# Performance work log

Hardware: AMD Instinct MI355X
Metric: run time of the kernel (lower is better)

## Reference

```python
import jax, jax.numpy as jnp
import numpy as np

B, C, H, W = 8, 32, 512, 512
WS = 8
CQ = C // 4                      # 8
N = (H // WS) * (W // WS)        # 4096 windows
ED = WS * WS * C                 # 2048 embed_dim
EPS = 1e-6


def setup_inputs() -> dict:
    key = jax.random.key(0)
    ks = jax.random.split(key, 16)
    s = 0.02
    return {
        "input_x": jax.random.normal(ks[0], (B, C, H, W), jnp.float32),
        # in_conv: Conv2d(C, C//4, 1)
        "w_in": jax.random.normal(ks[1], (CQ, C), jnp.float32) * s,
        "b_in": jnp.zeros((CQ,), jnp.float32),
        # conv: Conv2d(C, C//4, 1) + LayerNorm(C//4)
        "w_conv": jax.random.normal(ks[2], (CQ, C), jnp.float32) * s,
        "b_conv": jnp.zeros((CQ,), jnp.float32),
        "ln_w": jnp.ones((CQ,), jnp.float32),
        "ln_b": jnp.zeros((CQ,), jnp.float32),
        # out_CA: Conv2d(C//4, C, 1)
        "w_ca": jax.random.normal(ks[3], (C, CQ), jnp.float32) * s,
        "b_ca": jnp.zeros((C,), jnp.float32),
        # out_SA: Conv2d(C//4, 1, 3, pad 1)
        "w_sa": jax.random.normal(ks[4], (1, CQ, 3, 3), jnp.float32) * s,
        "b_sa": jnp.zeros((1,), jnp.float32),
        # out_mask MLP: Linear(ED, ED//2), Linear(ED//2, ED)  (torch weight [out,in])
        "w_m1": jax.random.normal(ks[5], (ED // 2, ED), jnp.float32) * s,
        "b_m1": jnp.zeros((ED // 2,), jnp.float32),
        "w_m2": jax.random.normal(ks[6], (ED, ED // 2), jnp.float32) * s,
        "b_m2": jnp.zeros((ED,), jnp.float32),
    }


def _leaky(x):
    return jax.nn.leaky_relu(x, 0.1)


def _conv1x1(x, w, b):
    # x: [B,Cin,H,W], w: [Cout,Cin]
    return jnp.einsum('bchw,oc->bohw', x, w) + b[None, :, None, None]


def reference(input_x, w_in, b_in, w_conv, b_conv, ln_w, ln_b,
              w_ca, b_ca, w_sa, b_sa, w_m1, b_m1, w_m2, b_m2):
    b_, c_, h_, w_ = input_x.shape
    n_win = (h_ // WS) * (w_ // WS)

    # in_conv branch
    x = _leaky(_conv1x1(input_x, w_in, b_in))          # [B,CQ,H,W]

    # conv branch: 1x1 conv -> channels_first LayerNorm -> leaky
    x_ = _conv1x1(input_x, w_conv, b_conv)             # [B,CQ,H,W]
    u = jnp.mean(x_, axis=1, keepdims=True)
    s = jnp.mean((x_ - u) ** 2, axis=1, keepdims=True)
    x_ = (x_ - u) / jnp.sqrt(s + EPS)
    x_ = _leaky(ln_w[None, :, None, None] * x_ + ln_b[None, :, None, None])

    # channel attention: global avg pool -> 1x1 conv -> sigmoid
    pooled = jnp.mean(x_, axis=(2, 3), keepdims=True)  # [B,CQ,1,1]
    ca = jax.nn.sigmoid(_conv1x1(pooled, w_ca, b_ca))  # [B,C,1,1]

    # spatial attention: 3x3 conv -> sigmoid
    sa = jax.lax.conv_general_dilated(
        x_, w_sa, (1, 1), 'SAME',
        dimension_numbers=('NCHW', 'OIHW', 'NCHW')) + b_sa[None, :, None, None]
    sa = jax.nn.sigmoid(sa)                            # [B,1,H,W]

    # window variance + bottom-k mask
    xm = jnp.mean(x, axis=1)                           # [B,H,W]
    xw = xm.reshape(b_, h_ // WS, WS, w_ // WS, WS)
    xw = xw.transpose(0, 1, 3, 2, 4).reshape(b_, n_win, WS * WS)  # [B,N,64]
    var_x = jnp.var(xw, axis=-1, ddof=1)               # [B,N] (torch unbiased var)
    k_top = n_win // 2
    _, idx = jax.lax.top_k(-var_x, k_top)              # indices of smallest-variance windows
    mask = jnp.ones((b_, n_win), input_x.dtype)
    mask = mask.at[jnp.arange(b_)[:, None], idx].set(0.0)  # vectorized scatter

    # broadcast 0/1 mask across embed dim, then MLP (see notes re: original bug)
    m = jnp.broadcast_to(mask[:, :, None], (b_, n_win, w_m1.shape[1]))
    hdd = _leaky(jnp.einsum('bnd,ed->bne', m, w_m1) + b_m1)
    out_mask = jnp.einsum('bne,fe->bnf', hdd, w_m2) + b_m2  # [B,N,ED]

    return (out_mask, ca, sa)
```

## Files before the change

kernel.cpp:

```cpp
#include <hip/hip_runtime.h>
#include <math.h>

#define B_   8
#define C_   32
#define H_   512
#define W_   512
#define CQ_  8
#define NW_  4096
#define ED_  2048
#define EH_  1024
#define EPS_ 1e-6f

#define AS1 __attribute__((address_space(1)))
#define AS3 __attribute__((address_space(3)))

__device__ __forceinline__ float leaky(float x) { return x > 0.f ? x : 0.1f * x; }
__device__ __forceinline__ float sigmoidf_(float x) { return 1.f / (1.f + __expf(-x)); }

__global__ __launch_bounds__(1024, 4) void pass_a(
    const float* __restrict__ x,
    const float* __restrict__ w_in, const float* __restrict__ b_in,
    const float* __restrict__ w_conv, const float* __restrict__ b_conv,
    const float* __restrict__ ln_w, const float* __restrict__ ln_b,
    float* __restrict__ xq_out,
    double* __restrict__ var_out,
    float* __restrict__ pooled_part)
{
    __shared__ float stage[3][4096];
    __shared__ float xm[4096];
    __shared__ float red[16][CQ_];

    const int tid  = threadIdx.x;
    const int band = blockIdx.x;
    const int b    = blockIdx.y;
    const int lane = tid & 63, wv = tid >> 6;
    const size_t plane = (size_t)H_ * W_;
    const float* xb = x + (size_t)b * C_ * plane;
    const float* gw = xb + (size_t)band * (8 * W_) + wv * 256 + lane * 4;

#define STAGE(buf, c)                                                          \
    __builtin_amdgcn_global_load_lds(                                          \
        (const AS1 unsigned int*)(gw + (size_t)(c) * plane),                   \
        (AS3 unsigned int*)(&stage[buf][wv * 256]), 16, 0, 0);

    float ycv[CQ_][4], yin[CQ_][4];
#pragma unroll
    for (int q = 0; q < CQ_; ++q)
#pragma unroll
        for (int j = 0; j < 4; ++j) { ycv[q][j] = 0.f; yin[q][j] = 0.f; }

    STAGE(0, 0) STAGE(1, 1) STAGE(2, 2)

#pragma unroll
    for (int c = 0; c < C_; ++c) {
        if (c < 30)       asm volatile("s_waitcnt vmcnt(2)" ::: "memory");
        else if (c == 30) asm volatile("s_waitcnt vmcnt(1)" ::: "memory");
        else              asm volatile("s_waitcnt vmcnt(0)" ::: "memory");
        asm volatile("s_barrier" ::: "memory");

        const float4 v = *reinterpret_cast<const float4*>(&stage[c % 3][tid * 4]);
#pragma unroll
        for (int q = 0; q < CQ_; ++q) {
            const float wc = w_conv[q * C_ + c];
            const float wi = w_in[q * C_ + c];
            ycv[q][0] = fmaf(wc, v.x, ycv[q][0]);
            ycv[q][1] = fmaf(wc, v.y, ycv[q][1]);
            ycv[q][2] = fmaf(wc, v.z, ycv[q][2]);
            ycv[q][3] = fmaf(wc, v.w, ycv[q][3]);
            yin[q][0] = fmaf(wi, v.x, yin[q][0]);
            yin[q][1] = fmaf(wi, v.y, yin[q][1]);
            yin[q][2] = fmaf(wi, v.z, yin[q][2]);
            yin[q][3] = fmaf(wi, v.w, yin[q][3]);
        }
        asm volatile("s_waitcnt lgkmcnt(0)" ::: "memory");
        asm volatile("s_barrier" ::: "memory");
        if (c + 3 < C_) { STAGE(c % 3, c + 3) }
    }
#undef STAGE

#pragma unroll
    for (int q = 0; q < CQ_; ++q) {
        const float bc = b_conv[q];
#pragma unroll
        for (int j = 0; j < 4; ++j) ycv[q][j] += bc;
    }

    float ps[CQ_];
#pragma unroll
    for (int q = 0; q < CQ_; ++q) ps[q] = 0.f;

    float xmv[4];
#pragma unroll
    for (int j = 0; j < 4; ++j) {
        float u = 0.f;
#pragma unroll
        for (int q = 0; q < CQ_; ++q) u += ycv[q][j];
        u *= 0.125f;
        float s = 0.f;
#pragma unroll
        for (int q = 0; q < CQ_; ++q) { const float d = ycv[q][j] - u; s = fmaf(d, d, s); }
        s *= 0.125f;
        const float inv = 1.f / sqrtf(s + EPS_);
        float m = 0.f;
#pragma unroll
        for (int q = 0; q < CQ_; ++q) {
            const float xv = leaky(fmaf(ln_w[q], (ycv[q][j] - u) * inv, ln_b[q]));
            ycv[q][j] = xv;
            ps[q] += xv;
            m += leaky(yin[q][j] + b_in[q]);
        }
        xmv[j] = m * 0.125f;
    }

    const int py = tid >> 7, px = (tid & 127) * 4;

#pragma unroll
    for (int q = 0; q < CQ_; ++q) {
        *reinterpret_cast<float4*>(
            &xq_out[(((size_t)b * CQ_ + q) * H_ + band * 8 + py) * W_ + px]) =
            make_float4(ycv[q][0], ycv[q][1], ycv[q][2], ycv[q][3]);
    }

    *reinterpret_cast<float4*>(&xm[tid * 4]) = make_float4(xmv[0], xmv[1], xmv[2], xmv[3]);

#pragma unroll
    for (int q = 0; q < CQ_; ++q) {
        float s = ps[q];
#pragma unroll
        for (int off = 32; off; off >>= 1) s += __shfl_xor(s, off);
        if (lane == 0) red[wv][q] = s;
    }

    __syncthreads();

    if (tid < CQ_) {
        float s = 0.f;
#pragma unroll
        for (int w = 0; w < 16; ++w) s += red[w][tid];
        const int bid = blockIdx.y * gridDim.x + blockIdx.x;
        pooled_part[bid * CQ_ + tid] = s;
    }

#pragma unroll
    for (int k = 0; k < 4; ++k) {
        const int win = wv * 4 + k;
        const double dv = (double)xm[(lane >> 3) * 512 + win * 8 + (lane & 7)];
        double s = dv;
#pragma unroll
        for (int off = 32; off; off >>= 1) s += __shfl_xor(s, off);
        const double mean = s * (1.0 / 64.0);
        const double d = dv - mean;
        double s2 = d * d;
#pragma unroll
        for (int off = 32; off; off >>= 1) s2 += __shfl_xor(s2, off);
        if (lane == 0) {
            const int n = band * 64 + win;
            var_out[(size_t)b * NW_ + n] = s2 * (1.0 / 63.0);
        }
    }
}

__global__ __launch_bounds__(256) void sa_kernel(
    const float* __restrict__ xq,
    const float* __restrict__ w_sa, const float* __restrict__ b_sa,
    float* __restrict__ sa_out)
{
    __shared__ float xl[CQ_][18][72];
    const int tid = threadIdx.x;
    const int b = blockIdx.z;
    const int ty = blockIdx.y * 16, tx = blockIdx.x * 64;

    for (int idx = tid; idx < CQ_ * 18 * 18; idx += 256) {
        const int ch = idx / 324;
        const int rem = idx % 324;
        const int r = rem / 18, c4 = rem % 18;
        const int gy = ty + r - 1;
        const int gxf = tx + c4 * 4 - 4;
        float4 v = make_float4(0.f, 0.f, 0.f, 0.f);
        if (gy >= 0 && gy < H_ && gxf >= 0 && gxf < W_)
            v = *reinterpret_cast<const float4*>(
                    &xq[(((size_t)b * CQ_ + ch) * H_ + gy) * W_ + gxf]);
        *reinterpret_cast<float4*>(&xl[ch][r][c4 * 4]) = v;
    }
    __syncthreads();

    const int px = (tid & 15) * 4, py = tid >> 4;
    const float bsa = b_sa[0];
    float acc[4] = {bsa, bsa, bsa, bsa};
#pragma unroll
    for (int q = 0; q < CQ_; ++q) {
#pragma unroll
        for (int dy = 0; dy < 3; ++dy) {
            const float* r = &xl[q][py + dy][px];
            const float4 aa = *reinterpret_cast<const float4*>(r);
            const float4 bb = *reinterpret_cast<const float4*>(r + 4);
            const float4 cc = *reinterpret_cast<const float4*>(r + 8);
            const float a[12] = {aa.x, aa.y, aa.z, aa.w, bb.x, bb.y, bb.z, bb.w,
                                 cc.x, cc.y, cc.z, cc.w};
#pragma unroll
            for (int dx = 0; dx < 3; ++dx) {
                const float w = w_sa[q * 9 + dy * 3 + dx];
#pragma unroll
                for (int j = 0; j < 4; ++j) acc[j] = fmaf(w, a[j + 3 + dx], acc[j]);
            }
        }
    }
    const float4 o = make_float4(sigmoidf_(acc[0]), sigmoidf_(acc[1]),
                                 sigmoidf_(acc[2]), sigmoidf_(acc[3]));
    *reinterpret_cast<float4*>(&sa_out[((size_t)b * H_ + (ty + py)) * W_ + tx + px]) = o;
}

__global__ __launch_bounds__(256) void k2_kernel(
    const double* __restrict__ var, float* __restrict__ maskF,
    const float* __restrict__ w_m1, const float* __restrict__ b_m1,
    float* __restrict__ h1, float* __restrict__ h0,
    const float* __restrict__ pooled_part,
    const float* __restrict__ w_ca, const float* __restrict__ b_ca,
    float* __restrict__ ca_out)
{
    __shared__ double sv[NW_];
    const int bi = blockIdx.x;
    const int tid = threadIdx.x;

    if (bi < 128) {
        const int b = bi >> 4;
        const double* vb = var + (size_t)b * NW_;
        for (int j = tid; j < NW_; j += 256) sv[j] = vb[j];
        __syncthreads();
        const int i = (bi & 15) * 256 + tid;
        const double vi = sv[i];
        int cnt = 0;
#pragma unroll 4
        for (int j = 0; j < NW_; ++j) {
            const double vj = sv[j];
            cnt += (vj < vi) || (vj == vi && j < i);
        }
        maskF[(size_t)b * NW_ + i] = (cnt < NW_ / 2) ? 0.f : 1.f;
    } else if (bi < 384) {
        const int wave = tid >> 6, lane = tid & 63;
        const int e = (bi - 128) * 4 + wave;
        const float* row = w_m1 + (size_t)e * ED_;
        float s = 0.f;
#pragma unroll
        for (int k = 0; k < ED_ / 64; ++k) s += row[lane + 64 * k];
#pragma unroll
        for (int off = 32; off; off >>= 1) s += __shfl_xor(s, off);
        if (lane == 0) {
            h1[e] = leaky(s + b_m1[e]);
            h0[e] = leaky(b_m1[e]);
        }
    } else {
        float* sp = (float*)sv;
        const int bq = tid >> 2, part = tid & 3;
        const int bb = bq >> 3, q = bq & 7;
        float s = 0.f;
        for (int k = part; k < 64; k += 4) s += pooled_part[((size_t)bb * 64 + k) * CQ_ + q];
        sp[tid] = s;
        __syncthreads();
        if (tid < 64)
            sp[256 + tid] = (sp[4 * tid] + sp[4 * tid + 1] + sp[4 * tid + 2] + sp[4 * tid + 3])
                            * (1.f / ((float)H_ * (float)W_));
        __syncthreads();
        const int ob = tid >> 5, o = tid & 31;
        float acc = b_ca[o];
#pragma unroll
        for (int qq = 0; qq < CQ_; ++qq)
            acc = fmaf(w_ca[o * CQ_ + qq], sp[256 + ob * CQ_ + qq], acc);
        ca_out[tid] = sigmoidf_(acc);
    }
}

__global__ __launch_bounds__(256) void o_kernel(const float* __restrict__ w_m2,
                                                const float* __restrict__ b_m2,
                                                const float* __restrict__ h1,
                                                const float* __restrict__ h0,
                                                float* __restrict__ o1, float* __restrict__ o0)
{
    const int wave = threadIdx.x >> 6, lane = threadIdx.x & 63;
    const int f = blockIdx.x * 4 + wave;
    const float* row = w_m2 + (size_t)f * EH_;
    float s1 = 0.f, s0 = 0.f;
#pragma unroll
    for (int k = 0; k < EH_ / 64; ++k) {
        const float w = row[lane + 64 * k];
        s1 = fmaf(w, h1[lane + 64 * k], s1);
        s0 = fmaf(w, h0[lane + 64 * k], s0);
    }
#pragma unroll
    for (int off = 32; off; off >>= 1) {
        s1 += __shfl_xor(s1, off);
        s0 += __shfl_xor(s0, off);
    }
    if (lane == 0) {
        o1[f] = s1 + b_m2[f];
        o0[f] = s0 + b_m2[f];
    }
}

__global__ __launch_bounds__(256) void bcast_kernel(const float* __restrict__ maskF,
                                                    const float* __restrict__ o1,
                                                    const float* __restrict__ o0,
                                                    float* __restrict__ out)
{
    __shared__ float sm[16];
    const int t = threadIdx.x;
    const long row0 = (long)blockIdx.x * 16;
    if (t < 16) sm[t] = maskF[row0 + t];
    const float4 a1 = ((const float4*)o1)[t], b1 = ((const float4*)o1)[t + 256];
    const float4 a0 = ((const float4*)o0)[t], b0 = ((const float4*)o0)[t + 256];
    __syncthreads();
#pragma unroll
    for (int r = 0; r < 16; ++r) {
        float4* dst = (float4*)(out + (size_t)(row0 + r) * ED_);
        const bool m = sm[r] > 0.5f;
        dst[t]       = m ? a1 : a0;
        dst[t + 256] = m ? b1 : b0;
    }
}

extern "C" void kernel_launch(void* const* d_in, const int* in_sizes, int n_in,
                              void* d_out, int out_size, void* d_ws, size_t ws_size,
                              hipStream_t stream)
{
    const float* x    = (const float*)d_in[0];
    const float* w_in = (const float*)d_in[1];
    const float* b_in = (const float*)d_in[2];
    const float* w_cv = (const float*)d_in[3];
    const float* b_cv = (const float*)d_in[4];
    const float* lnw  = (const float*)d_in[5];
    const float* lnb  = (const float*)d_in[6];
    const float* w_ca = (const float*)d_in[7];
    const float* b_ca = (const float*)d_in[8];
    const float* w_sa = (const float*)d_in[9];
    const float* b_sa = (const float*)d_in[10];
    const float* w_m1 = (const float*)d_in[11];
    const float* b_m1 = (const float*)d_in[12];
    const float* w_m2 = (const float*)d_in[13];
    const float* b_m2 = (const float*)d_in[14];

    float* out_mask = (float*)d_out;
    float* ca_out   = out_mask + (size_t)B_ * NW_ * ED_;
    float* sa_out   = ca_out + (size_t)B_ * C_;

    float* xq = out_mask;

    char* ws = (char*)d_ws;
    double* var       = (double*)ws;
    float*  maskF     = (float*)(ws + (size_t)B_ * NW_ * 8);
    float*  pooled_pp = maskF + (size_t)B_ * NW_;
    float*  h1 = pooled_pp + 512 * CQ_;
    float*  h0 = h1 + EH_;
    float*  o1 = h0 + EH_;
    float*  o0 = o1 + ED_;

    pass_a<<<dim3(64, B_), 1024, 0, stream>>>(
        x, w_in, b_in, w_cv, b_cv, lnw, lnb, xq, var, pooled_pp);
    sa_kernel<<<dim3(8, 32, B_), 256, 0, stream>>>(xq, w_sa, b_sa, sa_out);
    k2_kernel<<<385, 256, 0, stream>>>(var, maskF, w_m1, b_m1, h1, h0,
                                       pooled_pp, w_ca, b_ca, ca_out);
    o_kernel<<<ED_ / 4, 256, 0, stream>>>(w_m2, b_m2, h1, h0, o1, o0);
    bcast_kernel<<<B_ * NW_ / 16, 256, 0, stream>>>(maskF, o1, o0, out_mask);
}
```

Measured before the change: 345.3 us.

## Split pass_a into per-wave 8x32 tiles with deeper barrier-free LDS pipeline

Restructures pass_a from 1024-thread blocks covering a full 8-row band to 256-thread blocks covering 8x128 strips, with each wave owning its own 8x32 tile. Each wave now stages six channels ahead into a private LDS ring, so the block-wide barriers in the channel loop are no longer needed. Window variance is computed directly in registers with wave shuffles instead of through an LDS xm buffer. The pooled partials grow fourfold and the k2 reduction is adjusted to match. This trades a larger grid and more partial sums for more memory parallelism and less synchronisation on this bandwidth-bound pass.

```diff
diff --git a/kernel.cpp b/kernel.cpp
--- a/kernel.cpp
+++ b/kernel.cpp
@@ -17,7 +17,7 @@
 __device__ __forceinline__ float leaky(float x) { return x > 0.f ? x : 0.1f * x; }
 __device__ __forceinline__ float sigmoidf_(float x) { return 1.f / (1.f + __expf(-x)); }
 
-__global__ __launch_bounds__(1024, 4) void pass_a(
+__global__ __launch_bounds__(256) void pass_a(
     const float* __restrict__ x,
     const float* __restrict__ w_in, const float* __restrict__ b_in,
     const float* __restrict__ w_conv, const float* __restrict__ b_conv,
@@ -26,22 +26,25 @@
     double* __restrict__ var_out,
     float* __restrict__ pooled_part)
 {
-    __shared__ float stage[3][4096];
-    __shared__ float xm[4096];
-    __shared__ float red[16][CQ_];
+    __shared__ float stage[4][6][256];
+    __shared__ float red[4][CQ_];
 
     const int tid  = threadIdx.x;
-    const int band = blockIdx.x;
-    const int b    = blockIdx.y;
     const int lane = tid & 63, wv = tid >> 6;
+    const int sx   = blockIdx.x;
+    const int band = blockIdx.y;
+    const int b    = blockIdx.z;
     const size_t plane = (size_t)H_ * W_;
     const float* xb = x + (size_t)b * C_ * plane;
-    const float* gw = xb + (size_t)band * (8 * W_) + wv * 256 + lane * 4;
-
-#define STAGE(buf, c)                                                          \
+
+    const int row0 = band * 8 + (lane >> 3);
+    const int col0 = sx * 128 + wv * 32 + (lane & 7) * 4;
+    const float* gw = xb + (size_t)row0 * W_ + col0;
+
+#define STAGE(slot, c)                                                         \
     __builtin_amdgcn_global_load_lds(                                          \
         (const AS1 unsigned int*)(gw + (size_t)(c) * plane),                   \
-        (AS3 unsigned int*)(&stage[buf][wv * 256]), 16, 0, 0);
+        (AS3 unsigned int*)(&stage[wv][slot][0]), 16, 0, 0);
 
     float ycv[CQ_][4], yin[CQ_][4];
 #pragma unroll
@@ -49,16 +52,18 @@
 #pragma unroll
         for (int j = 0; j < 4; ++j) { ycv[q][j] = 0.f; yin[q][j] = 0.f; }
 
-    STAGE(0, 0) STAGE(1, 1) STAGE(2, 2)
+    STAGE(0, 0) STAGE(1, 1) STAGE(2, 2) STAGE(3, 3) STAGE(4, 4) STAGE(5, 5)
 
 #pragma unroll
     for (int c = 0; c < C_; ++c) {
-        if (c < 30)       asm volatile("s_waitcnt vmcnt(2)" ::: "memory");
+        if (c < 27)       asm volatile("s_waitcnt vmcnt(5)" ::: "memory");
+        else if (c == 27) asm volatile("s_waitcnt vmcnt(4)" ::: "memory");
+        else if (c == 28) asm volatile("s_waitcnt vmcnt(3)" ::: "memory");
+        else if (c == 29) asm volatile("s_waitcnt vmcnt(2)" ::: "memory");
         else if (c == 30) asm volatile("s_waitcnt vmcnt(1)" ::: "memory");
         else              asm volatile("s_waitcnt vmcnt(0)" ::: "memory");
-        asm volatile("s_barrier" ::: "memory");
-
-        const float4 v = *reinterpret_cast<const float4*>(&stage[c % 3][tid * 4]);
+
+        const float4 v = *reinterpret_cast<const float4*>(&stage[wv][c % 6][lane * 4]);
 #pragma unroll
         for (int q = 0; q < CQ_; ++q) {
             const float wc = w_conv[q * C_ + c];
@@ -72,9 +77,10 @@
             yin[q][2] = fmaf(wi, v.z, yin[q][2]);
             yin[q][3] = fmaf(wi, v.w, yin[q][3]);
         }
-        asm volatile("s_waitcnt lgkmcnt(0)" ::: "memory");
-        asm volatile("s_barrier" ::: "memory");
-        if (c + 3 < C_) { STAGE(c % 3, c + 3) }
+        if (c + 6 < C_) {
+            asm volatile("s_waitcnt lgkmcnt(0)" ::: "memory");
+            STAGE(c % 6, c + 6)
+        }
     }
 #undef STAGE
 
@@ -112,16 +118,36 @@
         xmv[j] = m * 0.125f;
     }
 
-    const int py = tid >> 7, px = (tid & 127) * 4;
-
 #pragma unroll
     for (int q = 0; q < CQ_; ++q) {
         *reinterpret_cast<float4*>(
-            &xq_out[(((size_t)b * CQ_ + q) * H_ + band * 8 + py) * W_ + px]) =
+            &xq_out[(((size_t)b * CQ_ + q) * H_ + row0) * W_ + col0]) =
             make_float4(ycv[q][0], ycv[q][1], ycv[q][2], ycv[q][3]);
     }
 
-    *reinterpret_cast<float4*>(&xm[tid * 4]) = make_float4(xmv[0], xmv[1], xmv[2], xmv[3]);
+    {
+        double s = (double)xmv[0] + (double)xmv[1] + (double)xmv[2] + (double)xmv[3];
+        s += __shfl_xor(s, 1);
+        s += __shfl_xor(s, 8);
+        s += __shfl_xor(s, 16);
+        s += __shfl_xor(s, 32);
+        const double mean = s * (1.0 / 64.0);
+        double s2 = 0.0;
+#pragma unroll
+        for (int j = 0; j < 4; ++j) {
+            const double d = (double)xmv[j] - mean;
+            s2 += d * d;
+        }
+        s2 += __shfl_xor(s2, 1);
+        s2 += __shfl_xor(s2, 8);
+        s2 += __shfl_xor(s2, 16);
+        s2 += __shfl_xor(s2, 32);
+        if ((lane >> 3) == 0 && (lane & 1) == 0) {
+            const int k = (lane & 7) >> 1;
+            const int n = band * 64 + sx * 16 + wv * 4 + k;
+            var_out[(size_t)b * NW_ + n] = s2 * (1.0 / 63.0);
+        }
+    }
 
 #pragma unroll
     for (int q = 0; q < CQ_; ++q) {
@@ -130,33 +156,11 @@
         for (int off = 32; off; off >>= 1) s += __shfl_xor(s, off);
         if (lane == 0) red[wv][q] = s;
     }
-
     __syncthreads();
-
     if (tid < CQ_) {
-        float s = 0.f;
-#pragma unroll
-        for (int w = 0; w < 16; ++w) s += red[w][tid];
-        const int bid = blockIdx.y * gridDim.x + blockIdx.x;
+        const float s = red[0][tid] + red[1][tid] + red[2][tid] + red[3][tid];
+        const int bid = ((int)blockIdx.z * 64 + blockIdx.y) * 4 + blockIdx.x;
         pooled_part[bid * CQ_ + tid] = s;
-    }
-
-#pragma unroll
-    for (int k = 0; k < 4; ++k) {
-        const int win = wv * 4 + k;
-        const double dv = (double)xm[(lane >> 3) * 512 + win * 8 + (lane & 7)];
-        double s = dv;
-#pragma unroll
-        for (int off = 32; off; off >>= 1) s += __shfl_xor(s, off);
-        const double mean = s * (1.0 / 64.0);
-        const double d = dv - mean;
-        double s2 = d * d;
-#pragma unroll
-        for (int off = 32; off; off >>= 1) s2 += __shfl_xor(s2, off);
-        if (lane == 0) {
-            const int n = band * 64 + win;
-            var_out[(size_t)b * NW_ + n] = s2 * (1.0 / 63.0);
-        }
     }
 }
 
@@ -254,7 +258,8 @@
         const int bq = tid >> 2, part = tid & 3;
         const int bb = bq >> 3, q = bq & 7;
         float s = 0.f;
-        for (int k = part; k < 64; k += 4) s += pooled_part[((size_t)bb * 64 + k) * CQ_ + q];
+        for (int k = part; k < 256; k += 4)
+            s += pooled_part[((size_t)bb * 256 + k) * CQ_ + q];
         sp[tid] = s;
         __syncthreads();
         if (tid < 64)
@@ -348,12 +353,12 @@
     double* var       = (double*)ws;
     float*  maskF     = (float*)(ws + (size_t)B_ * NW_ * 8);
     float*  pooled_pp = maskF + (size_t)B_ * NW_;
-    float*  h1 = pooled_pp + 512 * CQ_;
+    float*  h1 = pooled_pp + 2048 * CQ_;
     float*  h0 = h1 + EH_;
     float*  o1 = h0 + EH_;
     float*  o0 = o1 + ED_;
 
-    pass_a<<<dim3(64, B_), 1024, 0, stream>>>(
+    pass_a<<<dim3(4, 64, B_), 256, 0, stream>>>(
         x, w_in, b_in, w_cv, b_cv, lnw, lnb, xq, var, pooled_pp);
     sa_kernel<<<dim3(8, 32, B_), 256, 0, stream>>>(xq, w_sa, b_sa, sa_out);
     k2_kernel<<<385, 256, 0, stream>>>(var, maskF, w_m1, b_m1, h1, h0,
```

After: 324.9 us. 5.9% less time.

## Restructure pass_a into many small blocks with direct register loads

Applied to the files above, without the earlier changes.

Replaces the 512-block, 1024-thread pass_a (whole 8-row band per block, staged through LDS with global_load_lds triple buffering) with 8192 blocks of 256 threads. Each block handles an 8x32 tile of four windows, and each thread loads all 32 channels of one pixel straight into registers. Conv weights are staged once in LDS as interleaved float2 pairs, and block IDs are remapped across batches. This removes the per-channel barriers and gives more blocks for latency hiding. The cost is scalar (non-float4) loads and stores, and a pooled-partial array that grows to 8192 entries, which the ca reduction must now sum.

```diff
diff --git a/kernel.cpp b/kernel.cpp
--- a/kernel.cpp
+++ b/kernel.cpp
@@ -11,13 +11,10 @@
 #define EH_  1024
 #define EPS_ 1e-6f
 
-#define AS1 __attribute__((address_space(1)))
-#define AS3 __attribute__((address_space(3)))
-
 __device__ __forceinline__ float leaky(float x) { return x > 0.f ? x : 0.1f * x; }
 __device__ __forceinline__ float sigmoidf_(float x) { return 1.f / (1.f + __expf(-x)); }
 
-__global__ __launch_bounds__(1024, 4) void pass_a(
+__global__ __launch_bounds__(256, 8) void pass_a(
     const float* __restrict__ x,
     const float* __restrict__ w_in, const float* __restrict__ b_in,
     const float* __restrict__ w_conv, const float* __restrict__ b_conv,
@@ -26,135 +23,108 @@
     double* __restrict__ var_out,
     float* __restrict__ pooled_part)
 {
-    __shared__ float stage[3][4096];
-    __shared__ float xm[4096];
-    __shared__ float red[16][CQ_];
-
-    const int tid  = threadIdx.x;
-    const int band = blockIdx.x;
-    const int b    = blockIdx.y;
+    __shared__ float2 s_w[C_ * CQ_];
+    __shared__ float  xm[8][32];
+    __shared__ float  red[4][CQ_];
+
+    const int tid = threadIdx.x;
+    const int bid = blockIdx.x;
+    const int wl  = (bid & 7) * 1024 + (bid >> 3);
+    const int b    = wl >> 10;
+    const int rem  = wl & 1023;
+    const int band = rem >> 4;
+    const int sx   = rem & 15;
+
     const int lane = tid & 63, wv = tid >> 6;
     const size_t plane = (size_t)H_ * W_;
     const float* xb = x + (size_t)b * C_ * plane;
-    const float* gw = xb + (size_t)band * (8 * W_) + wv * 256 + lane * 4;
-
-#define STAGE(buf, c)                                                          \
-    __builtin_amdgcn_global_load_lds(                                          \
-        (const AS1 unsigned int*)(gw + (size_t)(c) * plane),                   \
-        (AS3 unsigned int*)(&stage[buf][wv * 256]), 16, 0, 0);
-
-    float ycv[CQ_][4], yin[CQ_][4];
+
+    {
+        const int c = tid >> 3, q = tid & 7;
+        s_w[tid] = make_float2(w_conv[q * C_ + c], w_in[q * C_ + c]);
+    }
+
+    const int row0 = band * 8 + (tid >> 5);
+    const int col0 = sx * 32 + (tid & 31);
+    const float* gp = xb + (size_t)row0 * W_ + col0;
+
+    float v[C_];
+#pragma unroll
+    for (int c = 0; c < C_; ++c) v[c] = gp[(size_t)c * plane];
+
+    __syncthreads();
+
+    float ycv[CQ_], yin[CQ_];
+#pragma unroll
+    for (int q = 0; q < CQ_; ++q) { ycv[q] = 0.f; yin[q] = 0.f; }
+
+#pragma unroll
+    for (int c = 0; c < C_; ++c) {
+        const float4 wA = *reinterpret_cast<const float4*>(&s_w[c * CQ_ + 0]);
+        const float4 wB = *reinterpret_cast<const float4*>(&s_w[c * CQ_ + 2]);
+        const float4 wC = *reinterpret_cast<const float4*>(&s_w[c * CQ_ + 4]);
+        const float4 wD = *reinterpret_cast<const float4*>(&s_w[c * CQ_ + 6]);
+        const float vc = v[c];
+        ycv[0] = fmaf(wA.x, vc, ycv[0]); yin[0] = fmaf(wA.y, vc, yin[0]);
+        ycv[1] = fmaf(wA.z, vc, ycv[1]); yin[1] = fmaf(wA.w, vc, yin[1]);
+        ycv[2] = fmaf(wB.x, vc, ycv[2]); yin[2] = fmaf(wB.y, vc, yin[2]);
+        ycv[3] = fmaf(wB.z, vc, ycv[3]); yin[3] = fmaf(wB.w, vc, yin[3]);
+        ycv[4] = fmaf(wC.x, vc, ycv[4]); yin[4] = fmaf(wC.y, vc, yin[4]);
+        ycv[5] = fmaf(wC.z, vc, ycv[5]); yin[5] = fmaf(wC.w, vc, yin[5]);
+        ycv[6] = fmaf(wD.x, vc, ycv[6]); yin[6] = fmaf(wD.y, vc, yin[6]);
+        ycv[7] = fmaf(wD.z, vc, ycv[7]); yin[7] = fmaf(wD.w, vc, yin[7]);
+    }
+
+    float u = 0.f;
+#pragma unroll
+    for (int q = 0; q < CQ_; ++q) { ycv[q] += b_conv[q]; u += ycv[q]; }
+    u *= 0.125f;
+    float s = 0.f;
+#pragma unroll
+    for (int q = 0; q < CQ_; ++q) { const float d = ycv[q] - u; s = fmaf(d, d, s); }
+    s *= 0.125f;
+    const float inv = 1.f / sqrtf(s + EPS_);
+    float m = 0.f;
+#pragma unroll
+    for (int q = 0; q < CQ_; ++q) {
+        const float xv = leaky(fmaf(ln_w[q], (ycv[q] - u) * inv, ln_b[q]));
+        ycv[q] = xv;
+        m += leaky(yin[q] + b_in[q]);
+    }
+    const float xmv = m * 0.125f;
+    xm[tid >> 5][tid & 31] = xmv;
+
 #pragma unroll
     for (int q = 0; q < CQ_; ++q)
-#pragma unroll
-        for (int j = 0; j < 4; ++j) { ycv[q][j] = 0.f; yin[q][j] = 0.f; }
-
-    STAGE(0, 0) STAGE(1, 1) STAGE(2, 2)
-
-#pragma unroll
-    for (int c = 0; c < C_; ++c) {
-        if (c < 30)       asm volatile("s_waitcnt vmcnt(2)" ::: "memory");
-        else if (c == 30) asm volatile("s_waitcnt vmcnt(1)" ::: "memory");
-        else              asm volatile("s_waitcnt vmcnt(0)" ::: "memory");
-        asm volatile("s_barrier" ::: "memory");
-
-        const float4 v = *reinterpret_cast<const float4*>(&stage[c % 3][tid * 4]);
-#pragma unroll
-        for (int q = 0; q < CQ_; ++q) {
-            const float wc = w_conv[q * C_ + c];
-            const float wi = w_in[q * C_ + c];
-            ycv[q][0] = fmaf(wc, v.x, ycv[q][0]);
-            ycv[q][1] = fmaf(wc, v.y, ycv[q][1]);
-            ycv[q][2] = fmaf(wc, v.z, ycv[q][2]);
-            ycv[q][3] = fmaf(wc, v.w, ycv[q][3]);
-            yin[q][0] = fmaf(wi, v.x, yin[q][0]);
-            yin[q][1] = fmaf(wi, v.y, yin[q][1]);
-            yin[q][2] = fmaf(wi, v.z, yin[q][2]);
-            yin[q][3] = fmaf(wi, v.w, yin[q][3]);
-        }
-        asm volatile("s_waitcnt lgkmcnt(0)" ::: "memory");
-        asm volatile("s_barrier" ::: "memory");
-        if (c + 3 < C_) { STAGE(c % 3, c + 3) }
-    }
-#undef STAGE
+        xq_out[(((size_t)b * CQ_ + q) * H_ + row0) * W_ + col0] = ycv[q];
 
 #pragma unroll
     for (int q = 0; q < CQ_; ++q) {
-        const float bc = b_conv[q];
-#pragma unroll
-        for (int j = 0; j < 4; ++j) ycv[q][j] += bc;
-    }
-
-    float ps[CQ_];
-#pragma unroll
-    for (int q = 0; q < CQ_; ++q) ps[q] = 0.f;
-
-    float xmv[4];
-#pragma unroll
-    for (int j = 0; j < 4; ++j) {
-        float u = 0.f;
-#pragma unroll
-        for (int q = 0; q < CQ_; ++q) u += ycv[q][j];
-        u *= 0.125f;
-        float s = 0.f;
-#pragma unroll
-        for (int q = 0; q < CQ_; ++q) { const float d = ycv[q][j] - u; s = fmaf(d, d, s); }
-        s *= 0.125f;
-        const float inv = 1.f / sqrtf(s + EPS_);
-        float m = 0.f;
-#pragma unroll
-        for (int q = 0; q < CQ_; ++q) {
-            const float xv = leaky(fmaf(ln_w[q], (ycv[q][j] - u) * inv, ln_b[q]));
-            ycv[q][j] = xv;
-            ps[q] += xv;
-            m += leaky(yin[q][j] + b_in[q]);
-        }
-        xmv[j] = m * 0.125f;
-    }
-
-    const int py = tid >> 7, px = (tid & 127) * 4;
-
-#pragma unroll
-    for (int q = 0; q < CQ_; ++q) {
-        *reinterpret_cast<float4*>(
-            &xq_out[(((size_t)b * CQ_ + q) * H_ + band * 8 + py) * W_ + px]) =
-            make_float4(ycv[q][0], ycv[q][1], ycv[q][2], ycv[q][3]);
-    }
-
-    *reinterpret_cast<float4*>(&xm[tid * 4]) = make_float4(xmv[0], xmv[1], xmv[2], xmv[3]);
-
-#pragma unroll
-    for (int q = 0; q < CQ_; ++q) {
-        float s = ps[q];
-#pragma unroll
-        for (int off = 32; off; off >>= 1) s += __shfl_xor(s, off);
-        if (lane == 0) red[wv][q] = s;
+        float ps = ycv[q];
+#pragma unroll
+        for (int off = 32; off; off >>= 1) ps += __shfl_xor(ps, off);
+        if (lane == 0) red[wv][q] = ps;
     }
 
     __syncthreads();
 
     if (tid < CQ_) {
-        float s = 0.f;
-#pragma unroll
-        for (int w = 0; w < 16; ++w) s += red[w][tid];
-        const int bid = blockIdx.y * gridDim.x + blockIdx.x;
-        pooled_part[bid * CQ_ + tid] = s;
-    }
-
-#pragma unroll
-    for (int k = 0; k < 4; ++k) {
-        const int win = wv * 4 + k;
-        const double dv = (double)xm[(lane >> 3) * 512 + win * 8 + (lane & 7)];
-        double s = dv;
-#pragma unroll
-        for (int off = 32; off; off >>= 1) s += __shfl_xor(s, off);
-        const double mean = s * (1.0 / 64.0);
+        const float t = red[0][tid] + red[1][tid] + red[2][tid] + red[3][tid];
+        pooled_part[(size_t)wl * CQ_ + tid] = t;
+    }
+
+    {
+        const double dv = (double)xm[lane >> 3][wv * 8 + (lane & 7)];
+        double t = dv;
+#pragma unroll
+        for (int off = 32; off; off >>= 1) t += __shfl_xor(t, off);
+        const double mean = t * (1.0 / 64.0);
         const double d = dv - mean;
         double s2 = d * d;
 #pragma unroll
         for (int off = 32; off; off >>= 1) s2 += __shfl_xor(s2, off);
         if (lane == 0) {
-            const int n = band * 64 + win;
+            const int n = band * 64 + sx * 4 + wv;
             var_out[(size_t)b * NW_ + n] = s2 * (1.0 / 63.0);
         }
     }
@@ -254,7 +224,8 @@
         const int bq = tid >> 2, part = tid & 3;
         const int bb = bq >> 3, q = bq & 7;
         float s = 0.f;
-        for (int k = part; k < 64; k += 4) s += pooled_part[((size_t)bb * 64 + k) * CQ_ + q];
+        for (int k = part; k < 1024; k += 4)
+            s += pooled_part[((size_t)bb * 1024 + k) * CQ_ + q];
         sp[tid] = s;
         __syncthreads();
         if (tid < 64)
@@ -348,12 +319,12 @@
     double* var       = (double*)ws;
     float*  maskF     = (float*)(ws + (size_t)B_ * NW_ * 8);
     float*  pooled_pp = maskF + (size_t)B_ * NW_;
-    float*  h1 = pooled_pp + 512 * CQ_;
+    float*  h1 = pooled_pp + 8192 * CQ_;
     float*  h0 = h1 + EH_;
     float*  o1 = h0 + EH_;
     float*  o0 = o1 + ED_;
 
-    pass_a<<<dim3(64, B_), 1024, 0, stream>>>(
+    pass_a<<<8192, 256, 0, stream>>>(
         x, w_in, b_in, w_cv, b_cv, lnw, lnb, xq, var, pooled_pp);
     sa_kernel<<<dim3(8, 32, B_), 256, 0, stream>>>(xq, w_sa, b_sa, sa_out);
     k2_kernel<<<385, 256, 0, stream>>>(var, maskF, w_m1, b_m1, h1, h0,
```

After: 486.1 us. 1.41x slower.
